# Kernel tuning notes

Hardware: AMD Instinct MI355X
Metric: run time of the kernel (lower is better)

The kernel has to match this reference:

```python
import jax, jax.numpy as jnp
import numpy as np

B, L, H, E = 4, 2048, 16, 64  # batch, seq, heads, head_dim (S=L, D=E)


def setup_inputs() -> dict:
    key = jax.random.key(0)
    kq, kk, kv = jax.random.split(key, 3)
    queries = jax.random.normal(kq, (B, L, H, E), dtype=jnp.float32)
    keys = jax.random.normal(kk, (B, L, H, E), dtype=jnp.float32)
    values = jax.random.normal(kv, (B, L, H, E), dtype=jnp.float32)
    return {"queries": queries, "keys": keys, "values": values}


def reference(queries, keys, values):
    Bq, Lq, Hq, Eq = queries.shape
    scale = 1.0 / float(np.sqrt(Eq))
    # scores: [B, H, L, S]
    scores = jnp.einsum('blhe,bshe->bhls', queries, keys)
    # causal mask: forbid attending to future positions (strict upper triangle)
    causal = jnp.triu(jnp.ones((Lq, Lq), dtype=bool), k=1)
    scores = jnp.where(causal[None, None, :, :], -jnp.inf, scores)
    A = jax.nn.softmax(scale * scores, axis=-1)  # dropout p=0 -> identity
    V = jnp.einsum('bhls,bshd->blhd', A, values)  # [B, L, H, D]
    return V
```

## Files before the change

### kernel.cpp

```cpp
#include <hip/hip_runtime.h>
#include <hip/hip_bf16.h>

typedef short bs8 __attribute__((ext_vector_type(8)));
typedef short bs4 __attribute__((ext_vector_type(4)));
typedef float f32x4 __attribute__((ext_vector_type(4)));
typedef float f32x16 __attribute__((ext_vector_type(16)));
typedef int i32x4 __attribute__((ext_vector_type(4)));

#define B_ 4
#define L_ 2048
#define H_ 16
#define E_ 64
#define KT_ 64
#define KSTR 72
#define SCSTR 68
#define NEG_INF (-1e30f)
#define SCALE_LOG2E (0.125f * 1.44269504088896340736f)

__device__ __forceinline__ short bf16of(float x) {
  __hip_bfloat16 h = __float2bfloat16(x);
  return *reinterpret_cast<short*>(&h);
}

__global__ __launch_bounds__(256) void prep(const float* __restrict__ K,
                                            const float* __restrict__ V,
                                            short* __restrict__ Kb,
                                            short* __restrict__ Vt) {
  __shared__ unsigned int lt[64 * 35];
  const int tid = threadIdx.x;
  if (blockIdx.x < 1024) {
    size_t base = (size_t)blockIdx.x * 256 + tid;
#pragma unroll
    for (int i = 0; i < 8; ++i) {
      size_t g = base + (size_t)i * 262144;
      int e4 = g & 15;
      int h  = (g >> 4) & 15;
      int s  = (g >> 8) & 2047;
      int b  = (int)(g >> 19);
      float4 v = *(const float4*)(K + g * 4);
      bs4 o;
      o.x = bf16of(v.x); o.y = bf16of(v.y); o.z = bf16of(v.z); o.w = bf16of(v.w);
      *(bs4*)(Kb + (((size_t)(b * 16 + h) * L_ + s) * E_ + e4 * 4)) = o;
    }
  } else {
    int vb = blockIdx.x - 1024;
    int st = vb & 31, bh = vb >> 5;
    int b = bh >> 4, h = bh & 15;
    int s0 = st * 64;
#pragma unroll
    for (int i = 0; i < 2; ++i) {
      int idx = i * 256 + tid;
      int sp = idx >> 4;
      int e4 = idx & 15;
      const float* p0 = V + (((size_t)b * L_ + s0 + 2 * sp) * H_ + h) * E_ + e4 * 4;
      float4 v0 = *(const float4*)p0;
      float4 v1 = *(const float4*)(p0 + H_ * E_);
      unsigned u;
      u = (unsigned short)bf16of(v0.x) | ((unsigned)(unsigned short)bf16of(v1.x) << 16);
      lt[(e4 * 4 + 0) * 35 + sp] = u;
      u = (unsigned short)bf16of(v0.y) | ((unsigned)(unsigned short)bf16of(v1.y) << 16);
      lt[(e4 * 4 + 1) * 35 + sp] = u;
      u = (unsigned short)bf16of(v0.z) | ((unsigned)(unsigned short)bf16of(v1.z) << 16);
      lt[(e4 * 4 + 2) * 35 + sp] = u;
      u = (unsigned short)bf16of(v0.w) | ((unsigned)(unsigned short)bf16of(v1.w) << 16);
      lt[(e4 * 4 + 3) * 35 + sp] = u;
    }
    __syncthreads();
#pragma unroll
    for (int i = 0; i < 2; ++i) {
      int idx = i * 256 + tid;
      int e  = idx >> 3;
      int s8 = idx & 7;
      uint4 o;
      o.x = lt[e * 35 + s8 * 4 + 0];
      o.y = lt[e * 35 + s8 * 4 + 1];
      o.z = lt[e * 35 + s8 * 4 + 2];
      o.w = lt[e * 35 + s8 * 4 + 3];
      *(uint4*)(Vt + ((size_t)bh * E_ + e) * L_ + s0 + 8 * s8) = o;
    }
  }
}

__global__ __launch_bounds__(256, 4) void flash_fwd(const float* __restrict__ Q,
                                                    const short* __restrict__ Kb,
                                                    const short* __restrict__ Vt,
                                                    float* __restrict__ O) {
  const int id  = blockIdx.x;
  const int xcd = id & 7;
  const int j   = id >> 3;
  const int bh  = xcd * 8 + (j >> 4);
  const int p   = j & 15;
  const int b = bh >> 4, h = bh & 15;
  const int tid = threadIdx.x;
  const int w = tid >> 6;
  const int g = w >> 1;
  const int s = w & 1;
  const int lane = tid & 63;
  const int l32 = lane & 31;
  const int hh  = lane >> 5;
  const int h8  = hh * 8;

  __shared__ __align__(16) char smem[18432];
  short* ldsK = (short*)smem;
  short* ldsV = (short*)(smem + KT_ * KSTR * 2);
  float* scb  = (float*)smem;

  const short* KbBase = Kb + (size_t)bh * L_ * E_;
  const short* VtBase = Vt + (size_t)bh * E_ * L_;

  const int sr = tid >> 3;
  const int sc8 = (tid & 7) * 8;

  for (int phase = 0; phase < 2; ++phase) {
    const int qt  = phase ? (31 - p) : p;
    const int q0w = qt * 64 + 32 * s;
    const int nkt = qt + 1;

    bs8 aQ[4];
    {
      const float* qp = Q + (((size_t)b * L_ + q0w + l32) * H_ + h) * E_ + h8;
#pragma unroll
      for (int ks = 0; ks < 4; ++ks) {
        float4 f0 = *(const float4*)(qp + ks * 16);
        float4 f1 = *(const float4*)(qp + ks * 16 + 4);
        bs8 a;
        a[0] = bf16of(f0.x * SCALE_LOG2E); a[1] = bf16of(f0.y * SCALE_LOG2E);
        a[2] = bf16of(f0.z * SCALE_LOG2E); a[3] = bf16of(f0.w * SCALE_LOG2E);
        a[4] = bf16of(f1.x * SCALE_LOG2E); a[5] = bf16of(f1.y * SCALE_LOG2E);
        a[6] = bf16of(f1.z * SCALE_LOG2E); a[7] = bf16of(f1.w * SCALE_LOG2E);
        aQ[ks] = a;
      }
    }

    f32x16 accO[2];
#pragma unroll
    for (int d = 0; d < 2; ++d)
#pragma unroll
      for (int r = 0; r < 16; ++r) accO[d][r] = 0.f;
    float accL = 0.f;

    bs8 pfK[2], pfV[2];
#pragma unroll
    for (int i = 0; i < 2; ++i) {
      pfK[i] = *(const bs8*)(KbBase + (size_t)(sr + 32 * i) * E_ + sc8);
      pfV[i] = *(const bs8*)(VtBase + (size_t)(sr + 32 * i) * L_ + sc8);
    }

    for (int kt = 0; kt < nkt; ++kt) {
      const int k0 = kt * KT_;
      __syncthreads();
#pragma unroll
      for (int i = 0; i < 2; ++i) {
        *(bs8*)&ldsK[(sr + 32 * i) * KSTR + sc8] = pfK[i];
        *(bs8*)&ldsV[(sr + 32 * i) * KSTR + sc8] = pfV[i];
      }
      if (kt + 1 < nkt) {
        const int kn = k0 + KT_;
#pragma unroll
        for (int i = 0; i < 2; ++i) {
          pfK[i] = *(const bs8*)(KbBase + (size_t)(kn + sr + 32 * i) * E_ + sc8);
          pfV[i] = *(const bs8*)(VtBase + (size_t)(sr + 32 * i) * L_ + kn + sc8);
        }
      }
      __syncthreads();

      const int kb = k0 + 32 * g;
      if (kb <= q0w + 31) {
        const bool diag = (kb + 31 > q0w);

        f32x16 cc;
#pragma unroll
        for (int r = 0; r < 16; ++r) cc[r] = 0.f;
        __builtin_amdgcn_s_setprio(1);
#pragma unroll
        for (int ks = 0; ks < 4; ++ks) {
          bs8 aK = *(const bs8*)&ldsK[(32 * g + l32) * KSTR + ks * 16 + h8];
          cc = __builtin_amdgcn_mfma_f32_32x32x16_bf16(aK, aQ[ks], cc, 0, 0, 0);
        }
        __builtin_amdgcn_s_setprio(0);
        if (diag) {
          const int qcol = q0w + l32;
#pragma unroll
          for (int r = 0; r < 16; ++r) {
            const int key = kb + ((r & 3) + 8 * (r >> 2) + 4 * hh);
            if (key > qcol) cc[r] = NEG_INF;
          }
        }
        float pv[16];
#pragma unroll
        for (int r = 0; r < 16; ++r) pv[r] = __builtin_amdgcn_exp2f(cc[r]);
        accL += ((((pv[0] + pv[1]) + (pv[2] + pv[3])) + ((pv[4] + pv[5]) + (pv[6] + pv[7]))) +
                 (((pv[8] + pv[9]) + (pv[10] + pv[11])) + ((pv[12] + pv[13]) + (pv[14] + pv[15]))));
        unsigned pk[8];
#pragma unroll
        for (int i = 0; i < 8; ++i)
          asm("v_cvt_pk_bf16_f32 %0, %1, %2"
              : "=v"(pk[i]) : "v"(pv[2 * i]), "v"(pv[2 * i + 1]));
        unsigned w0 = pk[0], w2 = pk[2];
        asm("v_permlane32_swap_b32 %0, %1" : "+v"(w0), "+v"(w2));
        unsigned w1 = pk[1], w3 = pk[3];
        asm("v_permlane32_swap_b32 %0, %1" : "+v"(w1), "+v"(w3));
        unsigned w4 = pk[4], w6 = pk[6];
        asm("v_permlane32_swap_b32 %0, %1" : "+v"(w4), "+v"(w6));
        unsigned w5 = pk[5], w7 = pk[7];
        asm("v_permlane32_swap_b32 %0, %1" : "+v"(w5), "+v"(w7));
        i32x4 f0 = {(int)w0, (int)w1, (int)w2, (int)w3};
        i32x4 f1 = {(int)w4, (int)w5, (int)w6, (int)w7};
        bs8 pB0 = *(bs8*)&f0;
        bs8 pB1 = *(bs8*)&f1;

        __builtin_amdgcn_s_setprio(1);
#pragma unroll
        for (int dsub = 0; dsub < 2; ++dsub) {
          bs8 aV0 = *(const bs8*)&ldsV[(dsub * 32 + l32) * KSTR + 32 * g + h8];
          bs8 aV1 = *(const bs8*)&ldsV[(dsub * 32 + l32) * KSTR + 32 * g + 16 + h8];
          accO[dsub] = __builtin_amdgcn_mfma_f32_32x32x16_bf16(aV0, pB0, accO[dsub], 0, 0, 0);
          accO[dsub] = __builtin_amdgcn_mfma_f32_32x32x16_bf16(aV1, pB1, accO[dsub], 0, 0, 0);
        }
        __builtin_amdgcn_s_setprio(0);
      }
    }

    const float Lf = accL + __shfl_xor(accL, 32, 64);
    __syncthreads();
    float* scbO = scb + s * (32 * SCSTR);
    float* scbL = scb + 2 * (32 * SCSTR) + s * 32;
    if (g == 1) {
#pragma unroll
      for (int dsub = 0; dsub < 2; ++dsub)
#pragma unroll
        for (int q4 = 0; q4 < 4; ++q4) {
          f32x4 vv = {accO[dsub][4 * q4 + 0], accO[dsub][4 * q4 + 1],
                      accO[dsub][4 * q4 + 2], accO[dsub][4 * q4 + 3]};
          *(f32x4*)&scbO[(size_t)l32 * SCSTR + dsub * 32 + 8 * q4 + 4 * hh] = vv;
        }
      if (hh == 0) scbL[l32] = Lf;
    }
    __syncthreads();
    if (g == 0) {
      const float inv = 1.f / (Lf + scbL[l32]);
#pragma unroll
      for (int dsub = 0; dsub < 2; ++dsub)
#pragma unroll
        for (int q4 = 0; q4 < 4; ++q4) {
          float* ptr = &scbO[(size_t)l32 * SCSTR + dsub * 32 + 8 * q4 + 4 * hh];
          f32x4 ov = *(const f32x4*)ptr;
          f32x4 vv = {(accO[dsub][4 * q4 + 0] + ov.x) * inv,
                      (accO[dsub][4 * q4 + 1] + ov.y) * inv,
                      (accO[dsub][4 * q4 + 2] + ov.z) * inv,
                      (accO[dsub][4 * q4 + 3] + ov.w) * inv};
          *(f32x4*)ptr = vv;
        }
#pragma unroll
      for (int jj = 0; jj < 8; ++jj) {
        const int qq = jj * 4 + (lane >> 4);
        const int d0 = (lane & 15) * 4;
        f32x4 ov = *(const f32x4*)&scbO[(size_t)qq * SCSTR + d0];
        float* op = O + (((size_t)b * L_ + qt * 64 + 32 * s + qq) * H_ + h) * E_ + d0;
        *(f32x4*)op = ov;
      }
    }
  }
}

extern "C" void kernel_launch(void* const* d_in, const int* in_sizes, int n_in,
                              void* d_out, int out_size, void* d_ws, size_t ws_size,
                              hipStream_t stream) {
  (void)in_sizes; (void)n_in; (void)out_size; (void)ws_size;
  const float* Q = (const float*)d_in[0];
  const float* K = (const float*)d_in[1];
  const float* V = (const float*)d_in[2];
  float* Out = (float*)d_out;
  short* Kb = (short*)d_ws;
  short* Vt = Kb + (size_t)B_ * H_ * L_ * E_;

  prep<<<1024 + 2048, 256, 0, stream>>>(K, V, Kb, Vt);
  flash_fwd<<<1024, 256, 0, stream>>>(Q, Kb, Vt, Out);
}
```

Before: 187.6 us.

## Fuse K/V bf16 prep into attention kernel with grid barrier and double-buffered LDS

Drops the separate prep launch. Each attention block now converts its own slice of K to bf16 and transposes its slice of V into workspace, then all blocks wait on a global atomic-counter barrier (reset by a memset every launch) before running attention. The K/V LDS tiles are also double-buffered, so each iteration needs one barrier instead of two and the next tile's stores overlap compute. The grid barrier assumes all 1024 blocks are resident at once; LDS use doubles, which could limit occupancy or deadlock if residency fails.

```diff
diff --git a/kernel.cpp b/kernel.cpp
--- a/kernel.cpp
+++ b/kernel.cpp
@@ -14,77 +14,27 @@
 #define KT_ 64
 #define KSTR 72
 #define SCSTR 68
+#define BUFB 18432
 #define NEG_INF (-1e30f)
 #define SCALE_LOG2E (0.125f * 1.44269504088896340736f)
+
+__device__ unsigned g_cnt;
 
 __device__ __forceinline__ short bf16of(float x) {
   __hip_bfloat16 h = __float2bfloat16(x);
   return *reinterpret_cast<short*>(&h);
 }
-
-__global__ __launch_bounds__(256) void prep(const float* __restrict__ K,
-                                            const float* __restrict__ V,
-                                            short* __restrict__ Kb,
-                                            short* __restrict__ Vt) {
-  __shared__ unsigned int lt[64 * 35];
-  const int tid = threadIdx.x;
-  if (blockIdx.x < 1024) {
-    size_t base = (size_t)blockIdx.x * 256 + tid;
-#pragma unroll
-    for (int i = 0; i < 8; ++i) {
-      size_t g = base + (size_t)i * 262144;
-      int e4 = g & 15;
-      int h  = (g >> 4) & 15;
-      int s  = (g >> 8) & 2047;
-      int b  = (int)(g >> 19);
-      float4 v = *(const float4*)(K + g * 4);
-      bs4 o;
-      o.x = bf16of(v.x); o.y = bf16of(v.y); o.z = bf16of(v.z); o.w = bf16of(v.w);
-      *(bs4*)(Kb + (((size_t)(b * 16 + h) * L_ + s) * E_ + e4 * 4)) = o;
-    }
-  } else {
-    int vb = blockIdx.x - 1024;
-    int st = vb & 31, bh = vb >> 5;
-    int b = bh >> 4, h = bh & 15;
-    int s0 = st * 64;
-#pragma unroll
-    for (int i = 0; i < 2; ++i) {
-      int idx = i * 256 + tid;
-      int sp = idx >> 4;
-      int e4 = idx & 15;
-      const float* p0 = V + (((size_t)b * L_ + s0 + 2 * sp) * H_ + h) * E_ + e4 * 4;
-      float4 v0 = *(const float4*)p0;
-      float4 v1 = *(const float4*)(p0 + H_ * E_);
-      unsigned u;
-      u = (unsigned short)bf16of(v0.x) | ((unsigned)(unsigned short)bf16of(v1.x) << 16);
-      lt[(e4 * 4 + 0) * 35 + sp] = u;
-      u = (unsigned short)bf16of(v0.y) | ((unsigned)(unsigned short)bf16of(v1.y) << 16);
-      lt[(e4 * 4 + 1) * 35 + sp] = u;
-      u = (unsigned short)bf16of(v0.z) | ((unsigned)(unsigned short)bf16of(v1.z) << 16);
-      lt[(e4 * 4 + 2) * 35 + sp] = u;
-      u = (unsigned short)bf16of(v0.w) | ((unsigned)(unsigned short)bf16of(v1.w) << 16);
-      lt[(e4 * 4 + 3) * 35 + sp] = u;
-    }
-    __syncthreads();
-#pragma unroll
-    for (int i = 0; i < 2; ++i) {
-      int idx = i * 256 + tid;
-      int e  = idx >> 3;
-      int s8 = idx & 7;
-      uint4 o;
-      o.x = lt[e * 35 + s8 * 4 + 0];
-      o.y = lt[e * 35 + s8 * 4 + 1];
-      o.z = lt[e * 35 + s8 * 4 + 2];
-      o.w = lt[e * 35 + s8 * 4 + 3];
-      *(uint4*)(Vt + ((size_t)bh * E_ + e) * L_ + s0 + 8 * s8) = o;
-    }
-  }
+__device__ __forceinline__ unsigned pk2(float lo, float hi) {
+  return (unsigned)(unsigned short)bf16of(lo) |
+         ((unsigned)(unsigned short)bf16of(hi) << 16);
 }
 
-__global__ __launch_bounds__(256, 4) void flash_fwd(const float* __restrict__ Q,
-                                                    const short* __restrict__ Kb,
-                                                    const short* __restrict__ Vt,
-                                                    float* __restrict__ O) {
+__global__ __launch_bounds__(256, 4) void fused(const float* __restrict__ Q,
+                                                const float* __restrict__ K,
+                                                const float* __restrict__ V,
+                                                short* __restrict__ Kb,
+                                                short* __restrict__ Vt,
+                                                float* __restrict__ O) {
   const int id  = blockIdx.x;
   const int xcd = id & 7;
   const int j   = id >> 3;
@@ -100,16 +50,65 @@
   const int hh  = lane >> 5;
   const int h8  = hh * 8;
 
-  __shared__ __align__(16) char smem[18432];
-  short* ldsK = (short*)smem;
-  short* ldsV = (short*)(smem + KT_ * KSTR * 2);
-  float* scb  = (float*)smem;
+  __shared__ __align__(16) char smem[2 * BUFB];
+
+  {
+    const int kr0 = p * 128;
+#pragma unroll
+    for (int i = 0; i < 8; ++i) {
+      const int gg = i * 256 + tid;
+      const int e4 = gg & 15, sloc = gg >> 4;
+      const int ss = kr0 + sloc;
+      float4 v = *(const float4*)(K + (((size_t)b * L_ + ss) * H_ + h) * E_ + e4 * 4);
+      bs4 o;
+      o.x = bf16of(v.x); o.y = bf16of(v.y); o.z = bf16of(v.z); o.w = bf16of(v.w);
+      *(bs4*)(Kb + ((size_t)bh * L_ + ss) * E_ + e4 * 4) = o;
+    }
+    unsigned* lt = (unsigned*)smem;
+    for (int ch = 0; ch < 2; ++ch) {
+      const int s0 = p * 128 + ch * 64;
+#pragma unroll
+      for (int i = 0; i < 2; ++i) {
+        const int idx = i * 256 + tid;
+        const int sp = idx >> 4, e4 = idx & 15;
+        const float* p0 = V + (((size_t)b * L_ + s0 + 2 * sp) * H_ + h) * E_ + e4 * 4;
+        float4 v0 = *(const float4*)p0;
+        float4 v1 = *(const float4*)(p0 + H_ * E_);
+        lt[(e4 * 4 + 0) * 35 + sp] = pk2(v0.x, v1.x);
+        lt[(e4 * 4 + 1) * 35 + sp] = pk2(v0.y, v1.y);
+        lt[(e4 * 4 + 2) * 35 + sp] = pk2(v0.z, v1.z);
+        lt[(e4 * 4 + 3) * 35 + sp] = pk2(v0.w, v1.w);
+      }
+      __syncthreads();
+#pragma unroll
+      for (int i = 0; i < 2; ++i) {
+        const int idx = i * 256 + tid;
+        const int e = idx >> 3, s8 = idx & 7;
+        uint4 o;
+        o.x = lt[e * 35 + s8 * 4 + 0];
+        o.y = lt[e * 35 + s8 * 4 + 1];
+        o.z = lt[e * 35 + s8 * 4 + 2];
+        o.w = lt[e * 35 + s8 * 4 + 3];
+        *(uint4*)(Vt + ((size_t)bh * E_ + e) * L_ + s0 + 8 * s8) = o;
+      }
+      __syncthreads();
+    }
+  }
+
+  __threadfence();
+  if (tid == 0) {
+    __hip_atomic_fetch_add(&g_cnt, 1u, __ATOMIC_ACQ_REL, __HIP_MEMORY_SCOPE_AGENT);
+    while (__hip_atomic_load(&g_cnt, __ATOMIC_ACQUIRE, __HIP_MEMORY_SCOPE_AGENT) < 1024u)
+      __builtin_amdgcn_s_sleep(2);
+  }
+  __syncthreads();
+  __threadfence();
 
   const short* KbBase = Kb + (size_t)bh * L_ * E_;
   const short* VtBase = Vt + (size_t)bh * E_ * L_;
-
   const int sr = tid >> 3;
   const int sc8 = (tid & 7) * 8;
+  float* scb = (float*)smem;
 
   for (int phase = 0; phase < 2; ++phase) {
     const int qt  = phase ? (31 - p) : p;
@@ -139,32 +138,54 @@
       for (int r = 0; r < 16; ++r) accO[d][r] = 0.f;
     float accL = 0.f;
 
+    __syncthreads();
     bs8 pfK[2], pfV[2];
 #pragma unroll
     for (int i = 0; i < 2; ++i) {
       pfK[i] = *(const bs8*)(KbBase + (size_t)(sr + 32 * i) * E_ + sc8);
       pfV[i] = *(const bs8*)(VtBase + (size_t)(sr + 32 * i) * L_ + sc8);
     }
+    {
+      short* nK = (short*)smem;
+      short* nV = (short*)(smem + 9216);
+#pragma unroll
+      for (int i = 0; i < 2; ++i) {
+        *(bs8*)&nK[(sr + 32 * i) * KSTR + sc8] = pfK[i];
+        *(bs8*)&nV[(sr + 32 * i) * KSTR + sc8] = pfV[i];
+      }
+    }
+    if (nkt > 1) {
+#pragma unroll
+      for (int i = 0; i < 2; ++i) {
+        pfK[i] = *(const bs8*)(KbBase + (size_t)(KT_ + sr + 32 * i) * E_ + sc8);
+        pfV[i] = *(const bs8*)(VtBase + (size_t)(sr + 32 * i) * L_ + KT_ + sc8);
+      }
+    }
+    __syncthreads();
+    int cur = 0;
 
     for (int kt = 0; kt < nkt; ++kt) {
-      const int k0 = kt * KT_;
-      __syncthreads();
-#pragma unroll
-      for (int i = 0; i < 2; ++i) {
-        *(bs8*)&ldsK[(sr + 32 * i) * KSTR + sc8] = pfK[i];
-        *(bs8*)&ldsV[(sr + 32 * i) * KSTR + sc8] = pfV[i];
-      }
+      short* cK = (short*)(smem + cur * BUFB);
+      short* cV = (short*)(smem + cur * BUFB + 9216);
       if (kt + 1 < nkt) {
-        const int kn = k0 + KT_;
+        short* nK = (short*)(smem + (cur ^ 1) * BUFB);
+        short* nV = (short*)(smem + (cur ^ 1) * BUFB + 9216);
 #pragma unroll
         for (int i = 0; i < 2; ++i) {
-          pfK[i] = *(const bs8*)(KbBase + (size_t)(kn + sr + 32 * i) * E_ + sc8);
-          pfV[i] = *(const bs8*)(VtBase + (size_t)(sr + 32 * i) * L_ + kn + sc8);
-        }
-      }
-      __syncthreads();
-
-      const int kb = k0 + 32 * g;
+          *(bs8*)&nK[(sr + 32 * i) * KSTR + sc8] = pfK[i];
+          *(bs8*)&nV[(sr + 32 * i) * KSTR + sc8] = pfV[i];
+        }
+        if (kt + 2 < nkt) {
+          const int kn = (kt + 2) * KT_;
+#pragma unroll
+          for (int i = 0; i < 2; ++i) {
+            pfK[i] = *(const bs8*)(KbBase + (size_t)(kn + sr + 32 * i) * E_ + sc8);
+            pfV[i] = *(const bs8*)(VtBase + (size_t)(sr + 32 * i) * L_ + kn + sc8);
+          }
+        }
+      }
+
+      const int kb = kt * KT_ + 32 * g;
       if (kb <= q0w + 31) {
         const bool diag = (kb + 31 > q0w);
 
@@ -174,7 +195,7 @@
         __builtin_amdgcn_s_setprio(1);
 #pragma unroll
         for (int ks = 0; ks < 4; ++ks) {
-          bs8 aK = *(const bs8*)&ldsK[(32 * g + l32) * KSTR + ks * 16 + h8];
+          bs8 aK = *(const bs8*)&cK[(32 * g + l32) * KSTR + ks * 16 + h8];
           cc = __builtin_amdgcn_mfma_f32_32x32x16_bf16(aK, aQ[ks], cc, 0, 0, 0);
         }
         __builtin_amdgcn_s_setprio(0);
@@ -212,17 +233,18 @@
         __builtin_amdgcn_s_setprio(1);
 #pragma unroll
         for (int dsub = 0; dsub < 2; ++dsub) {
-          bs8 aV0 = *(const bs8*)&ldsV[(dsub * 32 + l32) * KSTR + 32 * g + h8];
-          bs8 aV1 = *(const bs8*)&ldsV[(dsub * 32 + l32) * KSTR + 32 * g + 16 + h8];
+          bs8 aV0 = *(const bs8*)&cV[(dsub * 32 + l32) * KSTR + 32 * g + h8];
+          bs8 aV1 = *(const bs8*)&cV[(dsub * 32 + l32) * KSTR + 32 * g + 16 + h8];
           accO[dsub] = __builtin_amdgcn_mfma_f32_32x32x16_bf16(aV0, pB0, accO[dsub], 0, 0, 0);
           accO[dsub] = __builtin_amdgcn_mfma_f32_32x32x16_bf16(aV1, pB1, accO[dsub], 0, 0, 0);
         }
         __builtin_amdgcn_s_setprio(0);
       }
+      __syncthreads();
+      cur ^= 1;
     }
 
     const float Lf = accL + __shfl_xor(accL, 32, 64);
-    __syncthreads();
     float* scbO = scb + s * (32 * SCSTR);
     float* scbL = scb + 2 * (32 * SCSTR) + s * 32;
     if (g == 1) {
@@ -274,6 +296,8 @@
   short* Kb = (short*)d_ws;
   short* Vt = Kb + (size_t)B_ * H_ * L_ * E_;
 
-  prep<<<1024 + 2048, 256, 0, stream>>>(K, V, Kb, Vt);
-  flash_fwd<<<1024, 256, 0, stream>>>(Q, Kb, Vt, Out);
+  static void* cnt_addr = nullptr;
+  if (!cnt_addr) (void)hipGetSymbolAddress(&cnt_addr, HIP_SYMBOL(g_cnt));
+  hipMemsetAsync(cnt_addr, 0, sizeof(unsigned), stream);
+  fused<<<1024, 256, 0, stream>>>(Q, K, V, Kb, Vt, Out);
 }
```

After: 531.1 us. +183.1%, slower.

## Double-buffer K/V tiles in LDS to drop one barrier per iteration

Applied to the files above, without the earlier changes.

Turns the single LDS K/V tile buffer into two ping-pong buffers. Each iteration writes the next tile into the spare buffer and fetches the tile after that from global memory, then computes on the current buffer, so only one __syncthreads per key tile is needed instead of two. This doubles LDS use per block to 36 KB, which may cut occupancy, and adds a prologue that stages the first tile. The exp2 results now overwrite the score registers in place instead of a separate array, which is a minor register tidy-up.

```diff
diff --git a/kernel.cpp b/kernel.cpp
--- a/kernel.cpp
+++ b/kernel.cpp
@@ -14,6 +14,7 @@
 #define KT_ 64
 #define KSTR 72
 #define SCSTR 68
+#define BUFB 18432
 #define NEG_INF (-1e30f)
 #define SCALE_LOG2E (0.125f * 1.44269504088896340736f)
 
@@ -100,10 +101,8 @@
   const int hh  = lane >> 5;
   const int h8  = hh * 8;
 
-  __shared__ __align__(16) char smem[18432];
-  short* ldsK = (short*)smem;
-  short* ldsV = (short*)(smem + KT_ * KSTR * 2);
-  float* scb  = (float*)smem;
+  __shared__ __align__(16) char smem[2 * BUFB];
+  float* scb = (float*)smem;
 
   const short* KbBase = Kb + (size_t)bh * L_ * E_;
   const short* VtBase = Vt + (size_t)bh * E_ * L_;
@@ -139,32 +138,54 @@
       for (int r = 0; r < 16; ++r) accO[d][r] = 0.f;
     float accL = 0.f;
 
+    __syncthreads();
     bs8 pfK[2], pfV[2];
 #pragma unroll
     for (int i = 0; i < 2; ++i) {
       pfK[i] = *(const bs8*)(KbBase + (size_t)(sr + 32 * i) * E_ + sc8);
       pfV[i] = *(const bs8*)(VtBase + (size_t)(sr + 32 * i) * L_ + sc8);
     }
+    {
+      short* nK = (short*)smem;
+      short* nV = (short*)(smem + 9216);
+#pragma unroll
+      for (int i = 0; i < 2; ++i) {
+        *(bs8*)&nK[(sr + 32 * i) * KSTR + sc8] = pfK[i];
+        *(bs8*)&nV[(sr + 32 * i) * KSTR + sc8] = pfV[i];
+      }
+    }
+    if (nkt > 1) {
+#pragma unroll
+      for (int i = 0; i < 2; ++i) {
+        pfK[i] = *(const bs8*)(KbBase + (size_t)(KT_ + sr + 32 * i) * E_ + sc8);
+        pfV[i] = *(const bs8*)(VtBase + (size_t)(sr + 32 * i) * L_ + KT_ + sc8);
+      }
+    }
+    __syncthreads();
+    int cur = 0;
 
     for (int kt = 0; kt < nkt; ++kt) {
-      const int k0 = kt * KT_;
-      __syncthreads();
-#pragma unroll
-      for (int i = 0; i < 2; ++i) {
-        *(bs8*)&ldsK[(sr + 32 * i) * KSTR + sc8] = pfK[i];
-        *(bs8*)&ldsV[(sr + 32 * i) * KSTR + sc8] = pfV[i];
-      }
+      short* cK = (short*)(smem + cur * BUFB);
+      short* cV = (short*)(smem + cur * BUFB + 9216);
       if (kt + 1 < nkt) {
-        const int kn = k0 + KT_;
+        short* nK = (short*)(smem + (cur ^ 1) * BUFB);
+        short* nV = (short*)(smem + (cur ^ 1) * BUFB + 9216);
 #pragma unroll
         for (int i = 0; i < 2; ++i) {
-          pfK[i] = *(const bs8*)(KbBase + (size_t)(kn + sr + 32 * i) * E_ + sc8);
-          pfV[i] = *(const bs8*)(VtBase + (size_t)(sr + 32 * i) * L_ + kn + sc8);
-        }
-      }
-      __syncthreads();
-
-      const int kb = k0 + 32 * g;
+          *(bs8*)&nK[(sr + 32 * i) * KSTR + sc8] = pfK[i];
+          *(bs8*)&nV[(sr + 32 * i) * KSTR + sc8] = pfV[i];
+        }
+        if (kt + 2 < nkt) {
+          const int kn = (kt + 2) * KT_;
+#pragma unroll
+          for (int i = 0; i < 2; ++i) {
+            pfK[i] = *(const bs8*)(KbBase + (size_t)(kn + sr + 32 * i) * E_ + sc8);
+            pfV[i] = *(const bs8*)(VtBase + (size_t)(sr + 32 * i) * L_ + kn + sc8);
+          }
+        }
+      }
+
+      const int kb = kt * KT_ + 32 * g;
       if (kb <= q0w + 31) {
         const bool diag = (kb + 31 > q0w);
 
@@ -174,7 +195,7 @@
         __builtin_amdgcn_s_setprio(1);
 #pragma unroll
         for (int ks = 0; ks < 4; ++ks) {
-          bs8 aK = *(const bs8*)&ldsK[(32 * g + l32) * KSTR + ks * 16 + h8];
+          bs8 aK = *(const bs8*)&cK[(32 * g + l32) * KSTR + ks * 16 + h8];
           cc = __builtin_amdgcn_mfma_f32_32x32x16_bf16(aK, aQ[ks], cc, 0, 0, 0);
         }
         __builtin_amdgcn_s_setprio(0);
@@ -186,16 +207,15 @@
             if (key > qcol) cc[r] = NEG_INF;
           }
         }
-        float pv[16];
-#pragma unroll
-        for (int r = 0; r < 16; ++r) pv[r] = __builtin_amdgcn_exp2f(cc[r]);
-        accL += ((((pv[0] + pv[1]) + (pv[2] + pv[3])) + ((pv[4] + pv[5]) + (pv[6] + pv[7]))) +
-                 (((pv[8] + pv[9]) + (pv[10] + pv[11])) + ((pv[12] + pv[13]) + (pv[14] + pv[15]))));
+#pragma unroll
+        for (int r = 0; r < 16; ++r) cc[r] = __builtin_amdgcn_exp2f(cc[r]);
+        accL += ((((cc[0] + cc[1]) + (cc[2] + cc[3])) + ((cc[4] + cc[5]) + (cc[6] + cc[7]))) +
+                 (((cc[8] + cc[9]) + (cc[10] + cc[11])) + ((cc[12] + cc[13]) + (cc[14] + cc[15]))));
         unsigned pk[8];
 #pragma unroll
         for (int i = 0; i < 8; ++i)
           asm("v_cvt_pk_bf16_f32 %0, %1, %2"
-              : "=v"(pk[i]) : "v"(pv[2 * i]), "v"(pv[2 * i + 1]));
+              : "=v"(pk[i]) : "v"(cc[2 * i]), "v"(cc[2 * i + 1]));
         unsigned w0 = pk[0], w2 = pk[2];
         asm("v_permlane32_swap_b32 %0, %1" : "+v"(w0), "+v"(w2));
         unsigned w1 = pk[1], w3 = pk[3];
@@ -212,17 +232,18 @@
         __builtin_amdgcn_s_setprio(1);
 #pragma unroll
         for (int dsub = 0; dsub < 2; ++dsub) {
-          bs8 aV0 = *(const bs8*)&ldsV[(dsub * 32 + l32) * KSTR + 32 * g + h8];
-          bs8 aV1 = *(const bs8*)&ldsV[(dsub * 32 + l32) * KSTR + 32 * g + 16 + h8];
+          bs8 aV0 = *(const bs8*)&cV[(dsub * 32 + l32) * KSTR + 32 * g + h8];
+          bs8 aV1 = *(const bs8*)&cV[(dsub * 32 + l32) * KSTR + 32 * g + 16 + h8];
           accO[dsub] = __builtin_amdgcn_mfma_f32_32x32x16_bf16(aV0, pB0, accO[dsub], 0, 0, 0);
           accO[dsub] = __builtin_amdgcn_mfma_f32_32x32x16_bf16(aV1, pB1, accO[dsub], 0, 0, 0);
         }
         __builtin_amdgcn_s_setprio(0);
       }
+      __syncthreads();
+      cur ^= 1;
     }
 
     const float Lf = accL + __shfl_xor(accL, 32, 64);
-    __syncthreads();
     float* scbO = scb + s * (32 * SCSTR);
     float* scbL = scb + 2 * (32 * SCSTR) + s * 32;
     if (g == 1) {
```

New measurement: 194.1 us. +3.5%, slower.
